# Kernel optimization log

Measured on AMD Instinct MI355X. Metric: run time of the kernel, lower is better.

The kernel has to match this reference:

```python
import math
import jax, jax.numpy as jnp
import numpy as np

B, S, H, N = 2, 2048, 1024, 16
HN = H // N
ALPHA = 32.0


def setup_inputs() -> dict:
    key = jax.random.key(0)
    k1, k2, k3, k4, k5 = jax.random.split(key, 5)
    hidden_states = jax.random.normal(k1, (B, S, H), dtype=jnp.float32)
    # lower-triangular causal mask, broadcastable over batch and heads
    ltor_mask = jnp.tril(jnp.ones((S, S), dtype=jnp.float32))[None, None]
    w_qkv = jax.random.normal(k2, (H, 3 * H), dtype=jnp.float32) * 0.02
    b_qkv = jax.random.normal(k3, (3 * H,), dtype=jnp.float32) * 0.02
    w_dense = jax.random.normal(k4, (H, H), dtype=jnp.float32) * 0.02
    b_dense = jax.random.normal(k5, (H,), dtype=jnp.float32) * 0.02
    return {"hidden_states": hidden_states, "ltor_mask": ltor_mask,
            "w_qkv": w_qkv, "b_qkv": b_qkv, "w_dense": w_dense, "b_dense": b_dense}


def reference(hidden_states, ltor_mask, w_qkv, b_qkv, w_dense, b_dense):
    b, s, h = hidden_states.shape
    # fused QKV projection, split into q/k/v chunks along last dim
    qkv = hidden_states @ w_qkv + b_qkv            # [b, s, 3h]
    q, k, v = jnp.split(qkv, 3, axis=-1)
    # [b, s, h] -> [b, n, s, hn]
    def heads(t):
        return t.reshape(b, s, N, HN).transpose(0, 2, 1, 3)
    q, k, v = heads(q), heads(k), heads(v)
    # pb-relax: scale q before the matmul
    scores = jnp.einsum('bnqd,bnkd->bnqk', q / math.sqrt(HN), k)  # [b, n, s, s]
    mask = ltor_mask[:, :, -s:]                    # [1, 1, s, s]
    scores = scores * mask - 10000.0 * (1.0 - mask)
    # pb-relax max-subtraction stabilization (max over both score dims per head)
    ss = scores / ALPHA
    m = jax.lax.stop_gradient(jnp.max(ss.reshape(b, N, -1), axis=-1))[:, :, None, None]
    scores = (ss - m) * ALPHA
    probs = jax.nn.softmax(scores, axis=-1)        # dropout prob = 0
    ctx = jnp.einsum('bnqk,bnkd->bnqd', probs, v)  # [b, n, s, hn]
    ctx = ctx.transpose(0, 2, 1, 3).reshape(b, s, h)
    out = ctx @ w_dense + b_dense
    return out
```

## Files before the change

kernel.cpp:

```cpp
#include <hip/hip_runtime.h>
#include <hip/hip_bf16.h>
#include <stdint.h>

#define BB 2
#define SS 2048
#define HH 1024

typedef unsigned short u16;
typedef uint32_t u32;
typedef short bf8v __attribute__((ext_vector_type(8)));
typedef float f4 __attribute__((ext_vector_type(4)));

#define QSCALE 0.18033688011112042f

__device__ __forceinline__ u16 f2bf(float f) {
    u32 u = __builtin_bit_cast(u32, f);
    u = (u + 0x7fffu + ((u >> 16) & 1u)) >> 16;
    return (u16)u;
}

__device__ __forceinline__ u16 bfbits(float f) {
    return __builtin_bit_cast(u16, __float2bfloat16(f));
}

__device__ __forceinline__ void async16(const void* g, void* lds) {
    __builtin_amdgcn_global_load_lds(
        (const __attribute__((address_space(1))) u32*)g,
        (__attribute__((address_space(3))) u32*)lds, 16, 0, 0);
}

__global__ void cast_f32_bf16(const float* __restrict__ in, u16* __restrict__ out, int n) {
    int i = (blockIdx.x * blockDim.x + threadIdx.x) * 4;
    if (i < n) {
        float4 v = *(const float4*)(in + i);
        ushort4 o;
        o.x = f2bf(v.x); o.y = f2bf(v.y); o.z = f2bf(v.z); o.w = f2bf(v.w);
        *(ushort4*)(out + i) = o;
    }
}

__global__ void transpose_cast(const float* __restrict__ w, u16* __restrict__ wt, int K, int Nn) {
    __shared__ float tile[32][33];
    int tn = blockIdx.x, tk = blockIdx.y;
    int c = threadIdx.x & 31, r0 = threadIdx.x >> 5;
#pragma unroll
    for (int it = 0; it < 4; ++it) {
        int r = r0 + it * 8;
        tile[r][c] = w[(size_t)(tk * 32 + r) * Nn + tn * 32 + c];
    }
    __syncthreads();
#pragma unroll
    for (int it = 0; it < 4; ++it) {
        int r = r0 + it * 8;
        wt[(size_t)(tn * 32 + r) * K + tk * 32 + c] = f2bf(tile[c][r]);
    }
}

template<int EPI>
__global__ __launch_bounds__(256) void gemm_bt(
    const u16* __restrict__ A, const u16* __restrict__ Bt,
    const float* __restrict__ bias, void* __restrict__ Cout,
    int M, int N, int K)
{
    __shared__ __align__(16) u16 As[128 * 64];
    __shared__ __align__(16) u16 Bs[128 * 64];
    const int m0 = blockIdx.y * 128, n0 = blockIdx.x * 128;
    const int t = threadIdx.x, w = t >> 6, l = t & 63;
    const int wr = w >> 1, wc = w & 1;

    f4 acc[4][4];
#pragma unroll
    for (int i = 0; i < 4; ++i)
#pragma unroll
        for (int j = 0; j < 4; ++j) acc[i][j] = (f4){0.f, 0.f, 0.f, 0.f};

    const int nk = K >> 6;
    for (int kt = 0; kt < nk; ++kt) {
        const int k0 = kt << 6;
#pragma unroll
        for (int i = 0; i < 4; ++i) {
            int chunk = w * 256 + i * 64 + l;
            int row = chunk >> 3, seg = chunk & 7;
            int segg = seg ^ (row & 7);
            async16(A + (size_t)(m0 + row) * K + k0 + segg * 8,
                    (char*)As + (w * 256 + i * 64) * 16);
        }
#pragma unroll
        for (int i = 0; i < 4; ++i) {
            int chunk = w * 256 + i * 64 + l;
            int row = chunk >> 3, seg = chunk & 7;
            int segg = seg ^ (row & 7);
            async16(Bt + (size_t)(n0 + row) * K + k0 + segg * 8,
                    (char*)Bs + (w * 256 + i * 64) * 16);
        }
        __syncthreads();
#pragma unroll
        for (int kk = 0; kk < 2; ++kk) {
            bf8v af[4], bq[4];
#pragma unroll
            for (int fq = 0; fq < 4; ++fq) {
                int row = wr * 64 + fq * 16 + (l & 15);
                af[fq] = *(const bf8v*)((const char*)As +
                    ((row * 128 + kk * 64 + ((l >> 4) * 16)) ^ ((row & 7) << 4)));
            }
#pragma unroll
            for (int fr = 0; fr < 4; ++fr) {
                int row = wc * 64 + fr * 16 + (l & 15);
                bq[fr] = *(const bf8v*)((const char*)Bs +
                    ((row * 128 + kk * 64 + ((l >> 4) * 16)) ^ ((row & 7) << 4)));
            }
#pragma unroll
            for (int fq = 0; fq < 4; ++fq)
#pragma unroll
                for (int fr = 0; fr < 4; ++fr)
                    acc[fq][fr] = __builtin_amdgcn_mfma_f32_16x16x32_bf16(
                        af[fq], bq[fr], acc[fq][fr], 0, 0, 0);
        }
        __syncthreads();
    }
#pragma unroll
    for (int fq = 0; fq < 4; ++fq) {
#pragma unroll
        for (int fr = 0; fr < 4; ++fr) {
            int col = n0 + wc * 64 + fr * 16 + (l & 15);
            float bv = bias[col];
#pragma unroll
            for (int j = 0; j < 4; ++j) {
                int row = m0 + wr * 64 + fq * 16 + ((l >> 4) * 4) + j;
                float v = acc[fq][fr][j] + bv;
                if (EPI == 0) {
                    if (col < HH) v *= QSCALE;
                    ((u16*)Cout)[(size_t)row * N + col] = f2bf(v);
                } else {
                    ((float*)Cout)[(size_t)row * N + col] = v;
                }
            }
        }
    }
}

__global__ __launch_bounds__(256, 2) void attn_kernel(
    const u16* __restrict__ qkv,
    u16* __restrict__ ctx)
{
    __shared__ __align__(16) char sm[40960];

    const int bid = blockIdx.x;
    const int head = (bid & 7) * 4 + (bid >> 7);
    const int p    = (bid >> 3) & 15;
    const int b = head >> 4, n = head & 15;
    const int w = threadIdx.x >> 6, l = threadIdx.x & 63;
    const int q16 = l & 15, hi = l >> 4;
    const size_t rs = 3072;

    const int qtA = p, qtB = 31 - p;
    const int ntA = qtA + 1;

    const u16* kb0 = qkv + (size_t)(b * SS) * rs + HH + n * 64;
    const u16* vb0 = qkv + (size_t)(b * SS) * rs + 2 * HH + n * 64;

    const int m_   = (q16 & 7) << 4;
    const int krd0 = (q16 * 128 + hi * 16) ^ m_;
    const int krd1 = (q16 * 128 + 64 + hi * 16) ^ m_;
    const int psw  = 32768 + w * 2048;
    const int par0 = psw + krd0, par1 = psw + krd1;
    const int pstb = psw + q16 * 128;
    const int pst0 = pstb + ((0  + hi * 8) ^ m_);
    const int pst1 = pstb + ((32 + hi * 8) ^ m_);
    const int pst2 = pstb + ((64 + hi * 8) ^ m_);
    const int pst3 = pstb + ((96 + hi * 8) ^ m_);
    const int vwb  = 16384 + w * 2048 + (l >> 5) * 1024;
    const int vwl  = (l & 31) * 4;
    const int vrow2 = (l & 31) * 2, vcol = w * 16 + (l >> 5) * 8;

    auto stageK = [&](int kt, int buf) {
#pragma unroll
        for (int i = 0; i < 2; ++i) {
            int cbase = w * 128 + i * 64;
            int chunk = cbase + l;
            int row = chunk >> 3, seg = chunk & 7;
            int segg = seg ^ (row & 7);
            async16(kb0 + (size_t)(kt * 64 + row) * rs + segg * 8,
                    sm + buf * 8192 + cbase * 16);
        }
    };
    auto loadV = [&](int kt, bf8v& v0, bf8v& v1) {
        const u16* vp = vb0 + (size_t)(kt * 64 + vrow2) * rs + vcol;
        v0 = *(const bf8v*)vp;
        v1 = *(const bf8v*)(vp + rs);
    };
    auto writeVt = [&](int buf, bf8v v0, bf8v v1) {
        char* base = sm + vwb + buf * 8192;
#pragma unroll
        for (int j = 0; j < 8; ++j) {
            u32 pk = (u32)(u16)v0[j] | ((u32)(u16)v1[j] << 16);
            *(u32*)(base + j * 128 + (vwl ^ (j << 4))) = pk;
        }
    };

    {
        stageK(0, 0);
        bf8v v0c, v1c;
        loadV(0, v0c, v1c);
        writeVt(0, v0c, v1c);
    }
    __syncthreads();

    for (int phase = 0; phase < 2; ++phase) {
        const int qt = phase ? qtB : qtA;
        const int nt = phase ? (33 - ntA) : ntA;
        const int sbase = phase ? ntA : 0;

        bf8v q0, q1;
        {
            const u16* qp = qkv + (size_t)(b * SS + qt * 64 + w * 16 + q16) * rs + n * 64;
            q0 = *(const bf8v*)(qp + hi * 8);
            q1 = *(const bf8v*)(qp + 32 + hi * 8);
        }

        f4 o[4];
#pragma unroll
        for (int od = 0; od < 4; ++od) o[od] = (f4){0.f, 0.f, 0.f, 0.f};
        float lsum = 0.f;

        for (int kt = 0; kt < nt; ++kt) {
            const int s = sbase + kt;
            const int cur = s & 1, nx = cur ^ 1;
            const bool pf = (s + 1 < 33);
            bf8v nv0, nv1;
            if (pf) {
                const int s2 = s + 1;
                const int kt2 = (s2 >= ntA) ? (s2 - ntA) : s2;
                stageK(kt2, nx);
                loadV(kt2, nv0, nv1);
            }

            const int ka0 = krd0 + (cur << 13);
            const int ka1 = krd1 + (cur << 13);

            f4 sf[4];
#pragma unroll
            for (int fr = 0; fr < 4; ++fr) sf[fr] = (f4){0.f, 0.f, 0.f, 0.f};
            __builtin_amdgcn_s_setprio(1);
#pragma unroll
            for (int fr = 0; fr < 4; ++fr) {
                bf8v kf0 = *(const bf8v*)(sm + ka0 + fr * 2048);
                bf8v kf1 = *(const bf8v*)(sm + ka1 + fr * 2048);
                sf[fr] = __builtin_amdgcn_mfma_f32_16x16x32_bf16(kf0, q0, sf[fr], 0, 0, 0);
                sf[fr] = __builtin_amdgcn_mfma_f32_16x16x32_bf16(kf1, q1, sf[fr], 0, 0, 0);
            }
            __builtin_amdgcn_s_setprio(0);

            float pv[4][4];
#pragma unroll
            for (int fr = 0; fr < 4; ++fr)
#pragma unroll
                for (int j = 0; j < 4; ++j) pv[fr][j] = exp2f(sf[fr][j]);
            if (kt == nt - 1) {
                const int qloc = w * 16 + q16;
#pragma unroll
                for (int fr = 0; fr < 4; ++fr)
#pragma unroll
                    for (int j = 0; j < 4; ++j)
                        if (fr * 16 + hi * 4 + j > qloc) pv[fr][j] = 0.f;
            }
            float rsumL = 0.f;
#pragma unroll
            for (int fr = 0; fr < 4; ++fr)
#pragma unroll
                for (int j = 0; j < 4; ++j) rsumL += pv[fr][j];
            rsumL += __shfl_xor(rsumL, 16);
            rsumL += __shfl_xor(rsumL, 32);
            lsum += rsumL;

            {
                u32 a0 = (u32)bfbits(pv[0][0]) | ((u32)bfbits(pv[0][1]) << 16);
                u32 a1 = (u32)bfbits(pv[0][2]) | ((u32)bfbits(pv[0][3]) << 16);
                *(uint2*)(sm + pst0) = make_uint2(a0, a1);
                u32 b0 = (u32)bfbits(pv[1][0]) | ((u32)bfbits(pv[1][1]) << 16);
                u32 b1 = (u32)bfbits(pv[1][2]) | ((u32)bfbits(pv[1][3]) << 16);
                *(uint2*)(sm + pst1) = make_uint2(b0, b1);
                u32 c0 = (u32)bfbits(pv[2][0]) | ((u32)bfbits(pv[2][1]) << 16);
                u32 c1 = (u32)bfbits(pv[2][2]) | ((u32)bfbits(pv[2][3]) << 16);
                *(uint2*)(sm + pst2) = make_uint2(c0, c1);
                u32 d0 = (u32)bfbits(pv[3][0]) | ((u32)bfbits(pv[3][1]) << 16);
                u32 d1 = (u32)bfbits(pv[3][2]) | ((u32)bfbits(pv[3][3]) << 16);
                *(uint2*)(sm + pst3) = make_uint2(d0, d1);
            }

            __builtin_amdgcn_s_setprio(1);
#pragma unroll
            for (int kk = 0; kk < 2; ++kk) {
                bf8v pa = *(const bf8v*)(sm + (kk ? par1 : par0));
                const int kab = (kk ? ka1 : ka0) + 16384;
#pragma unroll
                for (int od = 0; od < 4; ++od) {
                    bf8v vf = *(const bf8v*)(sm + kab + od * 2048);
                    o[od] = __builtin_amdgcn_mfma_f32_16x16x32_bf16(pa, vf, o[od], 0, 0, 0);
                }
            }
            __builtin_amdgcn_s_setprio(0);

            if (pf) writeVt(nx, nv0, nv1);
            __syncthreads();
        }

        u16* cb = ctx + (size_t)(b * SS + qt * 64 + w * 16) * HH + n * 64;
#pragma unroll
        for (int j = 0; j < 4; ++j) {
            int qrow = hi * 4 + j;
            float inv = 1.0f / __shfl(lsum, qrow);
#pragma unroll
            for (int od = 0; od < 4; ++od) {
                int d = od * 16 + q16;
                cb[(size_t)qrow * HH + d] = f2bf(o[od][j] * inv);
            }
        }
    }
}

extern "C" void kernel_launch(void* const* d_in, const int* in_sizes, int n_in,
                              void* d_out, int out_size, void* d_ws, size_t ws_size,
                              hipStream_t stream)
{
    const float* hidden  = (const float*)d_in[0];
    const float* w_qkv   = (const float*)d_in[2];
    const float* b_qkv   = (const float*)d_in[3];
    const float* w_dense = (const float*)d_in[4];
    const float* b_dense = (const float*)d_in[5];

    u16* hid_bf = (u16*)d_ws;
    u16* wqkvT  = hid_bf + (size_t)4096 * 1024;
    u16* wdT    = wqkvT  + (size_t)3072 * 1024;
    u16* qkv_bf = wdT    + (size_t)1024 * 1024;
    u16* ctx_bf = hid_bf;

    cast_f32_bf16<<<4096, 256, 0, stream>>>(hidden, hid_bf, 4096 * 1024);
    transpose_cast<<<dim3(96, 32), 256, 0, stream>>>(w_qkv, wqkvT, 1024, 3072);
    transpose_cast<<<dim3(32, 32), 256, 0, stream>>>(w_dense, wdT, 1024, 1024);

    gemm_bt<0><<<dim3(24, 32), 256, 0, stream>>>(hid_bf, wqkvT, b_qkv, qkv_bf,
                                                 4096, 3072, 1024);
    attn_kernel<<<512, 256, 0, stream>>>(qkv_bf, ctx_bf);
    gemm_bt<1><<<dim3(8, 32), 256, 0, stream>>>(ctx_bf, wdT, b_dense, d_out,
                                                4096, 1024, 1024);
}
```

Before: 215.8 us.

## Deepen attention K/V pipeline to four LDS buffers with one barrier per tile

The two-phase attention loop becomes a single 33-step loop over a four-deep ring of K and V^T LDS buffers. K tiles are staged two steps ahead and V tiles are loaded into registers three steps ahead, with a manual vmcnt wait and a raw s_barrier in place of __syncthreads. Both Q tiles are loaded up front, and the first tile's epilogue runs mid-loop. LDS use grows from 40 KB to 72 KB, which may lower occupancy below the two blocks per CU requested, and the hand-counted vmcnt is fragile.

New measurement: 217.5 us. Within noise of the previous version (+0.8%).

```diff
diff --git a/kernel.cpp b/kernel.cpp
--- a/kernel.cpp
+++ b/kernel.cpp
@@ -143,7 +143,7 @@
     const u16* __restrict__ qkv,
     u16* __restrict__ ctx)
 {
-    __shared__ __align__(16) char sm[40960];
+    __shared__ __align__(16) char sm[73728];
 
     const int bid = blockIdx.x;
     const int head = (bid & 7) * 4 + (bid >> 7);
@@ -154,24 +154,26 @@
     const size_t rs = 3072;
 
     const int qtA = p, qtB = 31 - p;
-    const int ntA = qtA + 1;
+    const int ntA = p + 1;
 
     const u16* kb0 = qkv + (size_t)(b * SS) * rs + HH + n * 64;
-    const u16* vb0 = qkv + (size_t)(b * SS) * rs + 2 * HH + n * 64;
+    const u16* vbase = qkv + (size_t)(b * SS) * rs + 2 * HH + n * 64;
 
     const int m_   = (q16 & 7) << 4;
     const int krd0 = (q16 * 128 + hi * 16) ^ m_;
     const int krd1 = (q16 * 128 + 64 + hi * 16) ^ m_;
-    const int psw  = 32768 + w * 2048;
+    const int psw  = 65536 + w * 2048;
     const int par0 = psw + krd0, par1 = psw + krd1;
     const int pstb = psw + q16 * 128;
     const int pst0 = pstb + ((0  + hi * 8) ^ m_);
     const int pst1 = pstb + ((32 + hi * 8) ^ m_);
     const int pst2 = pstb + ((64 + hi * 8) ^ m_);
     const int pst3 = pstb + ((96 + hi * 8) ^ m_);
-    const int vwb  = 16384 + w * 2048 + (l >> 5) * 1024;
+    const int vwb  = 32768 + w * 2048 + (l >> 5) * 1024;
     const int vwl  = (l & 31) * 4;
     const int vrow2 = (l & 31) * 2, vcol = w * 16 + (l >> 5) * 8;
+
+    auto tl = [&](int gs) { return gs < ntA ? gs : gs - ntA; };
 
     auto stageK = [&](int kt, int buf) {
 #pragma unroll
@@ -185,7 +187,7 @@
         }
     };
     auto loadV = [&](int kt, bf8v& v0, bf8v& v1) {
-        const u16* vp = vb0 + (size_t)(kt * 64 + vrow2) * rs + vcol;
+        const u16* vp = vbase + (size_t)(kt * 64 + vrow2) * rs + vcol;
         v0 = *(const bf8v*)vp;
         v1 = *(const bf8v*)(vp + rs);
     };
@@ -198,125 +200,136 @@
         }
     };
 
+    bf8v qA0, qA1, qB0, qB1;
     {
-        stageK(0, 0);
-        bf8v v0c, v1c;
-        loadV(0, v0c, v1c);
-        writeVt(0, v0c, v1c);
-    }
-    __syncthreads();
-
-    for (int phase = 0; phase < 2; ++phase) {
-        const int qt = phase ? qtB : qtA;
-        const int nt = phase ? (33 - ntA) : ntA;
-        const int sbase = phase ? ntA : 0;
-
-        bf8v q0, q1;
-        {
-            const u16* qp = qkv + (size_t)(b * SS + qt * 64 + w * 16 + q16) * rs + n * 64;
-            q0 = *(const bf8v*)(qp + hi * 8);
-            q1 = *(const bf8v*)(qp + 32 + hi * 8);
-        }
-
-        f4 o[4];
-#pragma unroll
-        for (int od = 0; od < 4; ++od) o[od] = (f4){0.f, 0.f, 0.f, 0.f};
-        float lsum = 0.f;
-
-        for (int kt = 0; kt < nt; ++kt) {
-            const int s = sbase + kt;
-            const int cur = s & 1, nx = cur ^ 1;
-            const bool pf = (s + 1 < 33);
-            bf8v nv0, nv1;
-            if (pf) {
-                const int s2 = s + 1;
-                const int kt2 = (s2 >= ntA) ? (s2 - ntA) : s2;
-                stageK(kt2, nx);
-                loadV(kt2, nv0, nv1);
-            }
-
-            const int ka0 = krd0 + (cur << 13);
-            const int ka1 = krd1 + (cur << 13);
-
-            f4 sf[4];
-#pragma unroll
-            for (int fr = 0; fr < 4; ++fr) sf[fr] = (f4){0.f, 0.f, 0.f, 0.f};
-            __builtin_amdgcn_s_setprio(1);
-#pragma unroll
-            for (int fr = 0; fr < 4; ++fr) {
-                bf8v kf0 = *(const bf8v*)(sm + ka0 + fr * 2048);
-                bf8v kf1 = *(const bf8v*)(sm + ka1 + fr * 2048);
-                sf[fr] = __builtin_amdgcn_mfma_f32_16x16x32_bf16(kf0, q0, sf[fr], 0, 0, 0);
-                sf[fr] = __builtin_amdgcn_mfma_f32_16x16x32_bf16(kf1, q1, sf[fr], 0, 0, 0);
-            }
-            __builtin_amdgcn_s_setprio(0);
-
-            float pv[4][4];
-#pragma unroll
-            for (int fr = 0; fr < 4; ++fr)
-#pragma unroll
-                for (int j = 0; j < 4; ++j) pv[fr][j] = exp2f(sf[fr][j]);
-            if (kt == nt - 1) {
-                const int qloc = w * 16 + q16;
-#pragma unroll
-                for (int fr = 0; fr < 4; ++fr)
-#pragma unroll
-                    for (int j = 0; j < 4; ++j)
-                        if (fr * 16 + hi * 4 + j > qloc) pv[fr][j] = 0.f;
-            }
-            float rsumL = 0.f;
-#pragma unroll
-            for (int fr = 0; fr < 4; ++fr)
-#pragma unroll
-                for (int j = 0; j < 4; ++j) rsumL += pv[fr][j];
-            rsumL += __shfl_xor(rsumL, 16);
-            rsumL += __shfl_xor(rsumL, 32);
-            lsum += rsumL;
-
-            {
-                u32 a0 = (u32)bfbits(pv[0][0]) | ((u32)bfbits(pv[0][1]) << 16);
-                u32 a1 = (u32)bfbits(pv[0][2]) | ((u32)bfbits(pv[0][3]) << 16);
-                *(uint2*)(sm + pst0) = make_uint2(a0, a1);
-                u32 b0 = (u32)bfbits(pv[1][0]) | ((u32)bfbits(pv[1][1]) << 16);
-                u32 b1 = (u32)bfbits(pv[1][2]) | ((u32)bfbits(pv[1][3]) << 16);
-                *(uint2*)(sm + pst1) = make_uint2(b0, b1);
-                u32 c0 = (u32)bfbits(pv[2][0]) | ((u32)bfbits(pv[2][1]) << 16);
-                u32 c1 = (u32)bfbits(pv[2][2]) | ((u32)bfbits(pv[2][3]) << 16);
-                *(uint2*)(sm + pst2) = make_uint2(c0, c1);
-                u32 d0 = (u32)bfbits(pv[3][0]) | ((u32)bfbits(pv[3][1]) << 16);
-                u32 d1 = (u32)bfbits(pv[3][2]) | ((u32)bfbits(pv[3][3]) << 16);
-                *(uint2*)(sm + pst3) = make_uint2(d0, d1);
-            }
-
-            __builtin_amdgcn_s_setprio(1);
-#pragma unroll
-            for (int kk = 0; kk < 2; ++kk) {
-                bf8v pa = *(const bf8v*)(sm + (kk ? par1 : par0));
-                const int kab = (kk ? ka1 : ka0) + 16384;
-#pragma unroll
-                for (int od = 0; od < 4; ++od) {
-                    bf8v vf = *(const bf8v*)(sm + kab + od * 2048);
-                    o[od] = __builtin_amdgcn_mfma_f32_16x16x32_bf16(pa, vf, o[od], 0, 0, 0);
-                }
-            }
-            __builtin_amdgcn_s_setprio(0);
-
-            if (pf) writeVt(nx, nv0, nv1);
-            __syncthreads();
-        }
-
+        const u16* qp = qkv + (size_t)(b * SS + qtA * 64 + w * 16 + q16) * rs + n * 64;
+        qA0 = *(const bf8v*)(qp + hi * 8);
+        qA1 = *(const bf8v*)(qp + 32 + hi * 8);
+        const u16* qq = qkv + (size_t)(b * SS + qtB * 64 + w * 16 + q16) * rs + n * 64;
+        qB0 = *(const bf8v*)(qq + hi * 8);
+        qB1 = *(const bf8v*)(qq + 32 + hi * 8);
+    }
+
+    auto epi = [&](int qt, const f4* o, float lsum) {
         u16* cb = ctx + (size_t)(b * SS + qt * 64 + w * 16) * HH + n * 64;
 #pragma unroll
         for (int j = 0; j < 4; ++j) {
             int qrow = hi * 4 + j;
             float inv = 1.0f / __shfl(lsum, qrow);
 #pragma unroll
+            for (int od = 0; od < 4; ++od)
+                cb[(size_t)qrow * HH + od * 16 + q16] = f2bf(o[od][j] * inv);
+        }
+    };
+
+    stageK(tl(0), 0);
+    stageK(tl(1), 1);
+    bf8v t0, t1;  loadV(tl(0), t0, t1);
+    bf8v va0, va1; loadV(tl(1), va0, va1);
+    bf8v vc0, vc1; loadV(tl(2), vc0, vc1);
+    writeVt(0, t0, t1);
+
+    f4 o[4];
+#pragma unroll
+    for (int od = 0; od < 4; ++od) o[od] = (f4){0.f, 0.f, 0.f, 0.f};
+    float lsum = 0.f;
+    bf8v cq0 = qA0, cq1 = qA1;
+
+    for (int s = 0; s < 33; ++s) {
+        if (s == ntA) {
+            epi(qtA, o, lsum);
+#pragma unroll
+            for (int od = 0; od < 4; ++od) o[od] = (f4){0.f, 0.f, 0.f, 0.f};
+            lsum = 0.f;
+            cq0 = qB0; cq1 = qB1;
+        }
+
+        const int gk = (s + 2 <= 32) ? s + 2 : 32;
+        stageK(tl(gk), (s + 2) & 3);
+        if (s < 32) {
+            if ((s & 1) == 0) writeVt((s + 1) & 3, va0, va1);
+            else              writeVt((s + 1) & 3, vc0, vc1);
+        }
+        const int gv = (s + 3 <= 32) ? s + 3 : 32;
+        if ((s & 1) == 0) loadV(tl(gv), va0, va1);
+        else              loadV(tl(gv), vc0, vc1);
+
+        __builtin_amdgcn_sched_barrier(0);
+        asm volatile("s_waitcnt vmcnt(8) lgkmcnt(0)" ::: "memory");
+        __builtin_amdgcn_sched_barrier(0);
+        __builtin_amdgcn_s_barrier();
+        __builtin_amdgcn_sched_barrier(0);
+
+        const int cur = s & 3;
+        const int ka0 = krd0 + cur * 8192;
+        const int ka1 = krd1 + cur * 8192;
+
+        f4 sf[4];
+#pragma unroll
+        for (int fr = 0; fr < 4; ++fr) sf[fr] = (f4){0.f, 0.f, 0.f, 0.f};
+        __builtin_amdgcn_s_setprio(1);
+#pragma unroll
+        for (int fr = 0; fr < 4; ++fr) {
+            bf8v kf0 = *(const bf8v*)(sm + ka0 + fr * 2048);
+            bf8v kf1 = *(const bf8v*)(sm + ka1 + fr * 2048);
+            sf[fr] = __builtin_amdgcn_mfma_f32_16x16x32_bf16(kf0, cq0, sf[fr], 0, 0, 0);
+            sf[fr] = __builtin_amdgcn_mfma_f32_16x16x32_bf16(kf1, cq1, sf[fr], 0, 0, 0);
+        }
+        __builtin_amdgcn_s_setprio(0);
+
+        float pv[4][4];
+#pragma unroll
+        for (int fr = 0; fr < 4; ++fr)
+#pragma unroll
+            for (int j = 0; j < 4; ++j) pv[fr][j] = exp2f(sf[fr][j]);
+        if (s == ntA - 1 || s == 32) {
+            const int qloc = w * 16 + q16;
+#pragma unroll
+            for (int fr = 0; fr < 4; ++fr)
+#pragma unroll
+                for (int j = 0; j < 4; ++j)
+                    if (fr * 16 + hi * 4 + j > qloc) pv[fr][j] = 0.f;
+        }
+        float rsumL = 0.f;
+#pragma unroll
+        for (int fr = 0; fr < 4; ++fr)
+#pragma unroll
+            for (int j = 0; j < 4; ++j) rsumL += pv[fr][j];
+        rsumL += __shfl_xor(rsumL, 16);
+        rsumL += __shfl_xor(rsumL, 32);
+        lsum += rsumL;
+
+        {
+            u32 a0 = (u32)bfbits(pv[0][0]) | ((u32)bfbits(pv[0][1]) << 16);
+            u32 a1 = (u32)bfbits(pv[0][2]) | ((u32)bfbits(pv[0][3]) << 16);
+            *(uint2*)(sm + pst0) = make_uint2(a0, a1);
+            u32 b0 = (u32)bfbits(pv[1][0]) | ((u32)bfbits(pv[1][1]) << 16);
+            u32 b1 = (u32)bfbits(pv[1][2]) | ((u32)bfbits(pv[1][3]) << 16);
+            *(uint2*)(sm + pst1) = make_uint2(b0, b1);
+            u32 c0 = (u32)bfbits(pv[2][0]) | ((u32)bfbits(pv[2][1]) << 16);
+            u32 c1 = (u32)bfbits(pv[2][2]) | ((u32)bfbits(pv[2][3]) << 16);
+            *(uint2*)(sm + pst2) = make_uint2(c0, c1);
+            u32 d0 = (u32)bfbits(pv[3][0]) | ((u32)bfbits(pv[3][1]) << 16);
+            u32 d1 = (u32)bfbits(pv[3][2]) | ((u32)bfbits(pv[3][3]) << 16);
+            *(uint2*)(sm + pst3) = make_uint2(d0, d1);
+        }
+
+        __builtin_amdgcn_s_setprio(1);
+#pragma unroll
+        for (int kk = 0; kk < 2; ++kk) {
+            bf8v pa = *(const bf8v*)(sm + (kk ? par1 : par0));
+            const int vb_ = 32768 + cur * 8192 + (kk ? krd1 : krd0);
+#pragma unroll
             for (int od = 0; od < 4; ++od) {
-                int d = od * 16 + q16;
-                cb[(size_t)qrow * HH + d] = f2bf(o[od][j] * inv);
+                bf8v vf = *(const bf8v*)(sm + vb_ + od * 2048);
+                o[od] = __builtin_amdgcn_mfma_f32_16x16x32_bf16(pa, vf, o[od], 0, 0, 0);
             }
         }
-    }
+        __builtin_amdgcn_s_setprio(0);
+    }
+
+    asm volatile("s_waitcnt vmcnt(0)" ::: "memory");
+    epi(qtB, o, lsum);
 }
 
 extern "C" void kernel_launch(void* const* d_in, const int* in_sizes, int n_in,
```

## Split attention KV sweep across two blocks with atomic partial accumulation

Applied to the files above, without the earlier changes.

Each attention block's 33-tile key sweep (a paired short and long query tile) is split into two half-blocks, doubling the grid to 1024 blocks and raising the launch-bounds occupancy hint from 2 to 4. Partial outputs and row sums for the long query tile go into an fp32 scratch buffer through atomicAdd. A new norm kernel then divides and writes bf16 context. The goal is better occupancy and load balance on the attention kernel. The cost is an extra memset, atomic traffic, an extra kernel launch, and a workspace re-layout.

Result: no change. 215.7 us (-0.1%).

```diff
diff --git a/kernel.cpp b/kernel.cpp
--- a/kernel.cpp
+++ b/kernel.cpp
@@ -139,25 +139,30 @@
     }
 }
 
-__global__ __launch_bounds__(256, 2) void attn_kernel(
+__global__ __launch_bounds__(256, 4) void attn_kernel(
     const u16* __restrict__ qkv,
-    u16* __restrict__ ctx)
+    u16* __restrict__ ctx,
+    float* __restrict__ pO,
+    float* __restrict__ pL)
 {
     __shared__ __align__(16) char sm[40960];
 
     const int bid = blockIdx.x;
-    const int head = (bid & 7) * 4 + (bid >> 7);
+    const int head = (bid & 7) * 4 + (bid >> 8);
     const int p    = (bid >> 3) & 15;
+    const int h    = (bid >> 7) & 1;
     const int b = head >> 4, n = head & 15;
     const int w = threadIdx.x >> 6, l = threadIdx.x & 63;
     const int q16 = l & 15, hi = l >> 4;
     const size_t rs = 3072;
 
     const int qtA = p, qtB = 31 - p;
-    const int ntA = qtA + 1;
-
-    const u16* kb0 = qkv + (size_t)(b * SS) * rs + HH + n * 64;
-    const u16* vb0 = qkv + (size_t)(b * SS) * rs + 2 * HH + n * 64;
+    const int ntA = p + 1;
+    const int slot = head * 16 + (qtB - 16);
+    const int s0 = h ? 17 : 0, s1 = h ? 33 : 17;
+
+    const u16* kb0   = qkv + (size_t)(b * SS) * rs + HH + n * 64;
+    const u16* vbase = qkv + (size_t)(b * SS) * rs + 2 * HH + n * 64;
 
     const int m_   = (q16 & 7) << 4;
     const int krd0 = (q16 * 128 + hi * 16) ^ m_;
@@ -173,6 +178,8 @@
     const int vwl  = (l & 31) * 4;
     const int vrow2 = (l & 31) * 2, vcol = w * 16 + (l >> 5) * 8;
 
+    auto tl = [&](int gs) { return gs < ntA ? gs : gs - ntA; };
+
     auto stageK = [&](int kt, int buf) {
 #pragma unroll
         for (int i = 0; i < 2; ++i) {
@@ -185,7 +192,7 @@
         }
     };
     auto loadV = [&](int kt, bf8v& v0, bf8v& v1) {
-        const u16* vp = vb0 + (size_t)(kt * 64 + vrow2) * rs + vcol;
+        const u16* vp = vbase + (size_t)(kt * 64 + vrow2) * rs + vcol;
         v0 = *(const bf8v*)vp;
         v1 = *(const bf8v*)(vp + rs);
     };
@@ -198,124 +205,150 @@
         }
     };
 
+    bf8v qB0, qB1, cq0, cq1;
     {
-        stageK(0, 0);
+        const u16* qq = qkv + (size_t)(b * SS + qtB * 64 + w * 16 + q16) * rs + n * 64;
+        qB0 = *(const bf8v*)(qq + hi * 8);
+        qB1 = *(const bf8v*)(qq + 32 + hi * 8);
+    }
+    if (h == 0) {
+        const u16* qp = qkv + (size_t)(b * SS + qtA * 64 + w * 16 + q16) * rs + n * 64;
+        cq0 = *(const bf8v*)(qp + hi * 8);
+        cq1 = *(const bf8v*)(qp + 32 + hi * 8);
+    } else { cq0 = qB0; cq1 = qB1; }
+
+    {
+        stageK(tl(s0), s0 & 1);
         bf8v v0c, v1c;
-        loadV(0, v0c, v1c);
-        writeVt(0, v0c, v1c);
+        loadV(tl(s0), v0c, v1c);
+        writeVt(s0 & 1, v0c, v1c);
     }
     __syncthreads();
 
-    for (int phase = 0; phase < 2; ++phase) {
-        const int qt = phase ? qtB : qtA;
-        const int nt = phase ? (33 - ntA) : ntA;
-        const int sbase = phase ? ntA : 0;
-
-        bf8v q0, q1;
+    f4 o[4];
+#pragma unroll
+    for (int od = 0; od < 4; ++od) o[od] = (f4){0.f, 0.f, 0.f, 0.f};
+    float lsum = 0.f;
+
+    for (int s = s0; s < s1; ++s) {
+        if (h == 0 && s == ntA) {
+            u16* cb = ctx + (size_t)(b * SS + qtA * 64 + w * 16) * HH + n * 64;
+#pragma unroll
+            for (int j = 0; j < 4; ++j) {
+                int qrow = hi * 4 + j;
+                float inv = 1.0f / __shfl(lsum, qrow);
+#pragma unroll
+                for (int od = 0; od < 4; ++od)
+                    cb[(size_t)qrow * HH + od * 16 + q16] = f2bf(o[od][j] * inv);
+            }
+#pragma unroll
+            for (int od = 0; od < 4; ++od) o[od] = (f4){0.f, 0.f, 0.f, 0.f};
+            lsum = 0.f;
+            cq0 = qB0; cq1 = qB1;
+        }
+
+        const int cur = s & 1, nx = cur ^ 1;
+        const bool pf = (s + 1 < s1);
+        bf8v nv0, nv1;
+        if (pf) { stageK(tl(s + 1), nx); loadV(tl(s + 1), nv0, nv1); }
+
+        const int ka0 = krd0 + (cur << 13);
+        const int ka1 = krd1 + (cur << 13);
+
+        f4 sf[4];
+#pragma unroll
+        for (int fr = 0; fr < 4; ++fr) sf[fr] = (f4){0.f, 0.f, 0.f, 0.f};
+        __builtin_amdgcn_s_setprio(1);
+#pragma unroll
+        for (int fr = 0; fr < 4; ++fr) {
+            bf8v kf0 = *(const bf8v*)(sm + ka0 + fr * 2048);
+            bf8v kf1 = *(const bf8v*)(sm + ka1 + fr * 2048);
+            sf[fr] = __builtin_amdgcn_mfma_f32_16x16x32_bf16(kf0, cq0, sf[fr], 0, 0, 0);
+            sf[fr] = __builtin_amdgcn_mfma_f32_16x16x32_bf16(kf1, cq1, sf[fr], 0, 0, 0);
+        }
+        __builtin_amdgcn_s_setprio(0);
+
+        float pv[4][4];
+#pragma unroll
+        for (int fr = 0; fr < 4; ++fr)
+#pragma unroll
+            for (int j = 0; j < 4; ++j) pv[fr][j] = exp2f(sf[fr][j]);
+        if ((h == 0 && s == ntA - 1) || s == 32) {
+            const int qloc = w * 16 + q16;
+#pragma unroll
+            for (int fr = 0; fr < 4; ++fr)
+#pragma unroll
+                for (int j = 0; j < 4; ++j)
+                    if (fr * 16 + hi * 4 + j > qloc) pv[fr][j] = 0.f;
+        }
+        float rsumL = 0.f;
+#pragma unroll
+        for (int fr = 0; fr < 4; ++fr)
+#pragma unroll
+            for (int j = 0; j < 4; ++j) rsumL += pv[fr][j];
+        rsumL += __shfl_xor(rsumL, 16);
+        rsumL += __shfl_xor(rsumL, 32);
+        lsum += rsumL;
+
         {
-            const u16* qp = qkv + (size_t)(b * SS + qt * 64 + w * 16 + q16) * rs + n * 64;
-            q0 = *(const bf8v*)(qp + hi * 8);
-            q1 = *(const bf8v*)(qp + 32 + hi * 8);
-        }
-
-        f4 o[4];
-#pragma unroll
-        for (int od = 0; od < 4; ++od) o[od] = (f4){0.f, 0.f, 0.f, 0.f};
-        float lsum = 0.f;
-
-        for (int kt = 0; kt < nt; ++kt) {
-            const int s = sbase + kt;
-            const int cur = s & 1, nx = cur ^ 1;
-            const bool pf = (s + 1 < 33);
-            bf8v nv0, nv1;
-            if (pf) {
-                const int s2 = s + 1;
-                const int kt2 = (s2 >= ntA) ? (s2 - ntA) : s2;
-                stageK(kt2, nx);
-                loadV(kt2, nv0, nv1);
-            }
-
-            const int ka0 = krd0 + (cur << 13);
-            const int ka1 = krd1 + (cur << 13);
-
-            f4 sf[4];
-#pragma unroll
-            for (int fr = 0; fr < 4; ++fr) sf[fr] = (f4){0.f, 0.f, 0.f, 0.f};
-            __builtin_amdgcn_s_setprio(1);
-#pragma unroll
-            for (int fr = 0; fr < 4; ++fr) {
-                bf8v kf0 = *(const bf8v*)(sm + ka0 + fr * 2048);
-                bf8v kf1 = *(const bf8v*)(sm + ka1 + fr * 2048);
-                sf[fr] = __builtin_amdgcn_mfma_f32_16x16x32_bf16(kf0, q0, sf[fr], 0, 0, 0);
-                sf[fr] = __builtin_amdgcn_mfma_f32_16x16x32_bf16(kf1, q1, sf[fr], 0, 0, 0);
-            }
-            __builtin_amdgcn_s_setprio(0);
-
-            float pv[4][4];
-#pragma unroll
-            for (int fr = 0; fr < 4; ++fr)
-#pragma unroll
-                for (int j = 0; j < 4; ++j) pv[fr][j] = exp2f(sf[fr][j]);
-            if (kt == nt - 1) {
-                const int qloc = w * 16 + q16;
-#pragma unroll
-                for (int fr = 0; fr < 4; ++fr)
-#pragma unroll
-                    for (int j = 0; j < 4; ++j)
-                        if (fr * 16 + hi * 4 + j > qloc) pv[fr][j] = 0.f;
-            }
-            float rsumL = 0.f;
-#pragma unroll
-            for (int fr = 0; fr < 4; ++fr)
-#pragma unroll
-                for (int j = 0; j < 4; ++j) rsumL += pv[fr][j];
-            rsumL += __shfl_xor(rsumL, 16);
-            rsumL += __shfl_xor(rsumL, 32);
-            lsum += rsumL;
-
-            {
-                u32 a0 = (u32)bfbits(pv[0][0]) | ((u32)bfbits(pv[0][1]) << 16);
-                u32 a1 = (u32)bfbits(pv[0][2]) | ((u32)bfbits(pv[0][3]) << 16);
-                *(uint2*)(sm + pst0) = make_uint2(a0, a1);
-                u32 b0 = (u32)bfbits(pv[1][0]) | ((u32)bfbits(pv[1][1]) << 16);
-                u32 b1 = (u32)bfbits(pv[1][2]) | ((u32)bfbits(pv[1][3]) << 16);
-                *(uint2*)(sm + pst1) = make_uint2(b0, b1);
-                u32 c0 = (u32)bfbits(pv[2][0]) | ((u32)bfbits(pv[2][1]) << 16);
-                u32 c1 = (u32)bfbits(pv[2][2]) | ((u32)bfbits(pv[2][3]) << 16);
-                *(uint2*)(sm + pst2) = make_uint2(c0, c1);
-                u32 d0 = (u32)bfbits(pv[3][0]) | ((u32)bfbits(pv[3][1]) << 16);
-                u32 d1 = (u32)bfbits(pv[3][2]) | ((u32)bfbits(pv[3][3]) << 16);
-                *(uint2*)(sm + pst3) = make_uint2(d0, d1);
-            }
-
-            __builtin_amdgcn_s_setprio(1);
-#pragma unroll
-            for (int kk = 0; kk < 2; ++kk) {
-                bf8v pa = *(const bf8v*)(sm + (kk ? par1 : par0));
-                const int kab = (kk ? ka1 : ka0) + 16384;
-#pragma unroll
-                for (int od = 0; od < 4; ++od) {
-                    bf8v vf = *(const bf8v*)(sm + kab + od * 2048);
-                    o[od] = __builtin_amdgcn_mfma_f32_16x16x32_bf16(pa, vf, o[od], 0, 0, 0);
-                }
-            }
-            __builtin_amdgcn_s_setprio(0);
-
-            if (pf) writeVt(nx, nv0, nv1);
-            __syncthreads();
-        }
-
-        u16* cb = ctx + (size_t)(b * SS + qt * 64 + w * 16) * HH + n * 64;
-#pragma unroll
-        for (int j = 0; j < 4; ++j) {
-            int qrow = hi * 4 + j;
-            float inv = 1.0f / __shfl(lsum, qrow);
+            u32 a0 = (u32)bfbits(pv[0][0]) | ((u32)bfbits(pv[0][1]) << 16);
+            u32 a1 = (u32)bfbits(pv[0][2]) | ((u32)bfbits(pv[0][3]) << 16);
+            *(uint2*)(sm + pst0) = make_uint2(a0, a1);
+            u32 b0 = (u32)bfbits(pv[1][0]) | ((u32)bfbits(pv[1][1]) << 16);
+            u32 b1 = (u32)bfbits(pv[1][2]) | ((u32)bfbits(pv[1][3]) << 16);
+            *(uint2*)(sm + pst1) = make_uint2(b0, b1);
+            u32 c0 = (u32)bfbits(pv[2][0]) | ((u32)bfbits(pv[2][1]) << 16);
+            u32 c1 = (u32)bfbits(pv[2][2]) | ((u32)bfbits(pv[2][3]) << 16);
+            *(uint2*)(sm + pst2) = make_uint2(c0, c1);
+            u32 d0 = (u32)bfbits(pv[3][0]) | ((u32)bfbits(pv[3][1]) << 16);
+            u32 d1 = (u32)bfbits(pv[3][2]) | ((u32)bfbits(pv[3][3]) << 16);
+            *(uint2*)(sm + pst3) = make_uint2(d0, d1);
+        }
+
+        __builtin_amdgcn_s_setprio(1);
+#pragma unroll
+        for (int kk = 0; kk < 2; ++kk) {
+            bf8v pa = *(const bf8v*)(sm + (kk ? par1 : par0));
+            const int vb_ = 16384 + (cur << 13) + (kk ? krd1 : krd0);
 #pragma unroll
             for (int od = 0; od < 4; ++od) {
-                int d = od * 16 + q16;
-                cb[(size_t)qrow * HH + d] = f2bf(o[od][j] * inv);
-            }
-        }
+                bf8v vf = *(const bf8v*)(sm + vb_ + od * 2048);
+                o[od] = __builtin_amdgcn_mfma_f32_16x16x32_bf16(pa, vf, o[od], 0, 0, 0);
+            }
+        }
+        __builtin_amdgcn_s_setprio(0);
+
+        if (pf) writeVt(nx, nv0, nv1);
+        __syncthreads();
+    }
+
+    float* po = pO + (size_t)slot * 4096;
+#pragma unroll
+    for (int j = 0; j < 4; ++j) {
+        int qrow = w * 16 + hi * 4 + j;
+#pragma unroll
+        for (int od = 0; od < 4; ++od)
+            atomicAdd(po + qrow * 64 + od * 16 + q16, o[od][j]);
+    }
+    if (hi == 0) atomicAdd(pL + slot * 64 + w * 16 + q16, lsum);
+}
+
+__global__ __launch_bounds__(256) void norm_kernel(
+    const float* __restrict__ pO, const float* __restrict__ pL,
+    u16* __restrict__ ctx)
+{
+    const int slot = blockIdx.x;
+    const int head = slot >> 4;
+    const int qt = 16 + (slot & 15);
+    const int b = head >> 4, n = head & 15;
+    const float* po = pO + (size_t)slot * 4096;
+#pragma unroll
+    for (int i = 0; i < 16; ++i) {
+        int e = threadIdx.x + 256 * i;
+        int row = e >> 6, col = e & 63;
+        float v = po[e];
+        float lv = pL[slot * 64 + row];
+        ctx[(size_t)(b * SS + qt * 64 + row) * HH + n * 64 + col] = f2bf(v / lv);
     }
 }
 
@@ -329,11 +362,13 @@
     const float* w_dense = (const float*)d_in[4];
     const float* b_dense = (const float*)d_in[5];
 
-    u16* hid_bf = (u16*)d_ws;
+    u16* wdT    = (u16*)d_ws;
+    u16* ctx_bf = wdT + (size_t)1024 * 1024;
+    u16* qkv_bf = ctx_bf + (size_t)4096 * 1024;
+    u16* hid_bf = qkv_bf + (size_t)4096 * 3072;
     u16* wqkvT  = hid_bf + (size_t)4096 * 1024;
-    u16* wdT    = wqkvT  + (size_t)3072 * 1024;
-    u16* qkv_bf = wdT    + (size_t)1024 * 1024;
-    u16* ctx_bf = hid_bf;
+    float* pO   = (float*)hid_bf;
+    float* pL   = pO + (size_t)512 * 4096;
 
     cast_f32_bf16<<<4096, 256, 0, stream>>>(hidden, hid_bf, 4096 * 1024);
     transpose_cast<<<dim3(96, 32), 256, 0, stream>>>(w_qkv, wqkvT, 1024, 3072);
@@ -341,7 +376,9 @@
 
     gemm_bt<0><<<dim3(24, 32), 256, 0, stream>>>(hid_bf, wqkvT, b_qkv, qkv_bf,
                                                  4096, 3072, 1024);
-    attn_kernel<<<512, 256, 0, stream>>>(qkv_bf, ctx_bf);
+    hipMemsetAsync(pO, 0, (size_t)(512 * 4096 + 512 * 64) * 4, stream);
+    attn_kernel<<<1024, 256, 0, stream>>>(qkv_bf, ctx_bf, pO, pL);
+    norm_kernel<<<512, 256, 0, stream>>>(pO, pL, ctx_bf);
     gemm_bt<1><<<dim3(8, 32), 256, 0, stream>>>(ctx_bf, wdT, b_dense, d_out,
                                                 4096, 1024, 1024);
 }
```
